# Optimization experiments

Hardware: AMD Instinct MI355X
Metric: run time of the kernel (lower is better)

## Reference

```python
import jax, jax.numpy as jnp
import numpy as np

THRESHOLD = 10.0
K = 24
EPS = 1e-9
BN_EPS = 1e-5


def setup_inputs() -> dict:
    key = jax.random.key(0)
    k0, k1, k2, k3 = jax.random.split(key, 4)
    B, C, H, W = 4, 256, 64, 64
    x = jax.random.normal(k0, (B, C, H, W), jnp.float32)
    fc_w = jax.random.normal(k1, (C, C), jnp.float32) * (1.0 / np.sqrt(C))
    fc_b = jax.random.normal(k2, (C,), jnp.float32) * 0.01
    dist_w = jax.random.normal(k3, (64, C), jnp.float32) * (1.0 / np.sqrt(C))
    bn_gamma = jnp.ones((C,), jnp.float32)
    bn_beta = jnp.zeros((C,), jnp.float32)
    return {"x": x, "fc_w": fc_w, "fc_b": fc_b, "dist_w": dist_w,
            "bn_gamma": bn_gamma, "bn_beta": bn_beta}


def reference(x, fc_w, fc_b, dist_w, bn_gamma, bn_beta):
    B, C, H, W = x.shape
    N = H * W
    # ds branch: only triggers when H == 40; here H=64 so ds=1 (no pool/interp)
    x_flat = x.reshape(B, C, N).transpose(0, 2, 1)        # [B, N, C]
    # dist_embed: 1x1 conv == linear projection per spatial location
    emb = jnp.einsum('bnc,ec->bne', x_flat, dist_w)       # [B, N, 64]
    # pairwise Euclidean distances (cdist)
    sq = jnp.sum(emb * emb, axis=-1)                      # [B, N]
    d2 = sq[:, :, None] + sq[:, None, :] - 2.0 * jnp.einsum('bne,bme->bnm', emb, emb)
    dist = jnp.sqrt(jnp.clip(d2, 0.0))                    # [B, N, N]
    # kNN mask via top_k of -dist
    _, idx = jax.lax.top_k(-dist, K)                      # [B, N, K]
    bi = jnp.arange(B)[:, None, None]
    ni = jnp.arange(N)[None, :, None]
    knn_mask = jnp.zeros((B, N, N), bool).at[bi, ni, idx].set(True)
    adj = knn_mask & (dist <= THRESHOLD)
    adj = adj | jnp.eye(N, dtype=bool)[None]
    adj_f = adj.astype(x.dtype)                           # H: [B, N, E=N]
    # HypConv: X' = Dv^{-1} H De^{-1} H^T (X Theta), residual added outside
    X_lin = x_flat @ fc_w.T + fc_b                        # [B, N, C]
    Dv = jnp.clip(jnp.sum(adj_f, axis=2), EPS, None)      # [B, N]
    De = jnp.clip(jnp.sum(adj_f, axis=1), EPS, None)      # [B, E]
    H_De_inv = adj_f / De[:, None, :]
    S = (H_De_inv @ adj_f.transpose(0, 2, 1)) / Dv[:, :, None]   # [B, N, N]
    out_flat = S @ X_lin + x_flat                         # residual
    out = out_flat.transpose(0, 2, 1).reshape(B, C, H, W)
    # BatchNorm2d in training mode (batch statistics, biased variance)
    mean = jnp.mean(out, axis=(0, 2, 3))
    var = jnp.var(out, axis=(0, 2, 3))
    o = (out - mean[None, :, None, None]) * jax.lax.rsqrt(var[None, :, None, None] + BN_EPS)
    o = o * bn_gamma[None, :, None, None] + bn_beta[None, :, None, None]
    # SiLU
    return o * jax.nn.sigmoid(o)
```

## Files before the change

kernel.cpp:

```cpp
#include <hip/hip_runtime.h>

#define NB 4096
#define BATCH 4
#define CD 256
#define ED 64
#define KNN 24

typedef __attribute__((ext_vector_type(8))) short bf16x8;
typedef __attribute__((ext_vector_type(4))) float f32x4;

__device__ __forceinline__ unsigned short f2bf(float x) {
  unsigned u = __float_as_uint(x);
  unsigned r = (u + 0x7fffu + ((u >> 16) & 1u)) >> 16;
  return (unsigned short)r;
}

__global__ __launch_bounds__(256) void k_emb(const float* __restrict__ x,
                                             const float* __restrict__ dist_w,
                                             unsigned* __restrict__ emb_hl,
                                             float* __restrict__ sq,
                                             unsigned* __restrict__ thr_g) {
  __shared__ float wds[ED * CD];
  __shared__ float red[64 * 4];
  const int b = blockIdx.x >> 6;
  const int n0 = (blockIdx.x & 63) << 6;
  const int tid = threadIdx.x;
  const float4* wsrc = (const float4*)dist_w;
  float4* wdst = (float4*)wds;
#pragma unroll
  for (int k = 0; k < 16; ++k) wdst[tid + 256 * k] = wsrc[tid + 256 * k];
  __syncthreads();
  const int eg = tid >> 6;
  const int nl = tid & 63;
  const int n = n0 + nl;
  float acc[16];
#pragma unroll
  for (int t = 0; t < 16; ++t) acc[t] = 0.f;
  const float* xb = x + (size_t)b * CD * NB + n;
#pragma unroll 2
  for (int c4 = 0; c4 < CD; c4 += 4) {
    float x0 = xb[(size_t)(c4 + 0) * NB];
    float x1 = xb[(size_t)(c4 + 1) * NB];
    float x2 = xb[(size_t)(c4 + 2) * NB];
    float x3 = xb[(size_t)(c4 + 3) * NB];
#pragma unroll
    for (int t = 0; t < 16; ++t) {
      float4 wv = *(const float4*)&wds[(eg * 16 + t) * CD + c4];
      acc[t] = fmaf(x0, wv.x, acc[t]);
      acc[t] = fmaf(x1, wv.y, acc[t]);
      acc[t] = fmaf(x2, wv.z, acc[t]);
      acc[t] = fmaf(x3, wv.w, acc[t]);
    }
  }
  float s = 0.f;
#pragma unroll
  for (int t = 0; t < 16; ++t) s = fmaf(acc[t], acc[t], s);
  unsigned hw[8], lw[8];
#pragma unroll
  for (int i = 0; i < 8; ++i) {
    unsigned short h0 = f2bf(acc[2 * i]);
    unsigned short h1 = f2bf(acc[2 * i + 1]);
    float l0f = acc[2 * i] - __uint_as_float((unsigned)h0 << 16);
    float l1f = acc[2 * i + 1] - __uint_as_float((unsigned)h1 << 16);
    hw[i] = (unsigned)h0 | ((unsigned)h1 << 16);
    lw[i] = (unsigned)f2bf(l0f) | ((unsigned)f2bf(l1f) << 16);
  }
  uint4* g = (uint4*)emb_hl;
  const size_t gb = ((size_t)(b * NB + n)) * 16;
  const int k15 = n & 15;
  g[gb + ((2 * eg) ^ k15)]     = make_uint4(hw[0], hw[1], hw[2], hw[3]);
  g[gb + ((2 * eg + 1) ^ k15)] = make_uint4(hw[4], hw[5], hw[6], hw[7]);
  g[gb + ((8 + 2 * eg) ^ k15)]     = make_uint4(lw[0], lw[1], lw[2], lw[3]);
  g[gb + ((8 + 2 * eg + 1) ^ k15)] = make_uint4(lw[4], lw[5], lw[6], lw[7]);
  red[nl * 4 + eg] = s;
  __syncthreads();
  if (tid < 64) {
    sq[b * NB + n0 + tid] = red[tid * 4] + red[tid * 4 + 1] + red[tid * 4 + 2] + red[tid * 4 + 3];
    thr_g[(b << 12) + n0 + tid] = 0x42C80000u;
  }
}

__global__ __launch_bounds__(256) void k_xlin(const float* __restrict__ x,
                                              const float* __restrict__ fc_w,
                                              const float* __restrict__ fc_b,
                                              float* __restrict__ xlin) {
  __shared__ float xt[64 * 64];
  __shared__ float wt[64 * 260];
  const int b = blockIdx.x >> 6;
  const int n0 = (blockIdx.x & 63) << 6;
  const int tid = threadIdx.x;
  const int nl4 = tid & 15;
  const int cg = tid >> 4;
  float acc[4][16];
#pragma unroll
  for (int i = 0; i < 4; ++i)
#pragma unroll
    for (int j = 0; j < 16; ++j) acc[i][j] = 0.f;

  for (int kt = 0; kt < 4; ++kt) {
    __syncthreads();
#pragma unroll 4
    for (int i = 0; i < 16; ++i) {
      int idx = tid + 256 * i;
      int k = idx >> 6, n = idx & 63;
      xt[idx] = x[((size_t)(b * CD + kt * 64 + k)) * NB + n0 + n];
    }
#pragma unroll 4
    for (int i = 0; i < 16; ++i) {
      int q = tid + 256 * i;
      int c = q >> 4, k4 = (q & 15) * 4;
      float4 v = *(const float4*)&fc_w[(size_t)c * CD + kt * 64 + k4];
      wt[(k4 + 0) * 260 + c] = v.x;
      wt[(k4 + 1) * 260 + c] = v.y;
      wt[(k4 + 2) * 260 + c] = v.z;
      wt[(k4 + 3) * 260 + c] = v.w;
    }
    __syncthreads();
#pragma unroll 2
    for (int k = 0; k < 64; ++k) {
      float4 xv = *(const float4*)&xt[k * 64 + 4 * nl4];
#pragma unroll
      for (int j = 0; j < 4; ++j) {
        float4 wv = *(const float4*)&wt[k * 260 + 4 * cg + 64 * j];
        const float* wp = &wv.x;
#pragma unroll
        for (int l = 0; l < 4; ++l) {
          acc[0][4 * j + l] = fmaf(xv.x, wp[l], acc[0][4 * j + l]);
          acc[1][4 * j + l] = fmaf(xv.y, wp[l], acc[1][4 * j + l]);
          acc[2][4 * j + l] = fmaf(xv.z, wp[l], acc[2][4 * j + l]);
          acc[3][4 * j + l] = fmaf(xv.w, wp[l], acc[3][4 * j + l]);
        }
      }
    }
  }
#pragma unroll
  for (int i = 0; i < 4; ++i) {
    int n = n0 + 4 * nl4 + i;
    float* dst = xlin + ((size_t)(b * NB + n)) * CD;
#pragma unroll
    for (int j = 0; j < 4; ++j) {
      int c = 4 * cg + 64 * j;
      float4 bv = *(const float4*)&fc_b[c];
      float4 o;
      o.x = acc[i][4 * j + 0] + bv.x;
      o.y = acc[i][4 * j + 1] + bv.y;
      o.z = acc[i][4 * j + 2] + bv.z;
      o.w = acc[i][4 * j + 3] + bv.w;
      *(float4*)&dst[c] = o;
    }
  }
}

__global__ __launch_bounds__(512, 4) void k_distp(const unsigned* __restrict__ emb_hl,
                                                  const float* __restrict__ sq,
                                                  unsigned* __restrict__ thr_g,
                                                  unsigned long long* __restrict__ part) {
  __shared__ __align__(16) unsigned char smem[78592];
  unsigned* eN = (unsigned*)smem;
  unsigned* eM = (unsigned*)(smem + 16384);
  float* sqN   = (float*)(smem + 32768);
  float* sqMp  = (float*)(smem + 33024);
  int* hist    = (int*)(smem + 35072);
  int* collectK= (int*)(smem + 51456);
  int* cnt     = (int*)(smem + 51712);
  unsigned long long* cand = (unsigned long long*)(smem + 51968);

  const int bid = blockIdx.x;
  const int mp = bid & 7;
  const int nt = (bid >> 3) & 63;
  const int b  = bid >> 9;
  const int n0 = nt << 6;
  const int m00 = mp << 9;
  const int tid = threadIdx.x;
  const uint4* embg = (const uint4*)emb_hl;
  const size_t bbase = (size_t)b * NB;
  const int gbase = (b << 12) + n0;

#pragma unroll
  for (int k = 0; k < 2; ++k) {
    int q = tid + 512 * k;
    int r = q >> 4, ch = q & 15;
    *(uint4*)&eN[r * 64 + ch * 4] = embg[(bbase + n0 + r) * 16 + ch];
  }
  if (tid < 64) sqN[tid] = sq[b * NB + n0 + tid];
  sqMp[tid] = sq[b * NB + m00 + tid];
#pragma unroll
  for (int i = 0; i < 8; ++i) hist[tid + 512 * i] = 0;

  const int w = tid >> 6, lane = tid & 63;
  const int quad = lane >> 4, lr = lane & 15;
  const int rt = w >> 1;
  const int ct0 = (w & 1) * 2;
  const int rowA = rt * 16 + lr;
  const int rA = tid >> 4, chA = tid & 15;
  const int rB = rA + 32;

  uint4 pf0, pf1;

#define CHUNK_MFMA(m0_)                                                            \
  f32x4 acc0 = {0.f, 0.f, 0.f, 0.f};                                               \
  f32x4 acc1 = {0.f, 0.f, 0.f, 0.f};                                               \
  _Pragma("unroll")                                                                \
  for (int kk = 0; kk < 2; ++kk) {                                                 \
    const int cb = quad + 4 * kk;                                                  \
    bf16x8 a_hi = *(const bf16x8*)&eN[rowA * 64 + ((cb) ^ lr) * 4];                \
    bf16x8 a_lo = *(const bf16x8*)&eN[rowA * 64 + ((cb + 8) ^ lr) * 4];            \
    int rowB0 = ct0 * 16 + lr, rowB1 = rowB0 + 16;                                 \
    bf16x8 b0_hi = *(const bf16x8*)&eM[rowB0 * 64 + ((cb) ^ lr) * 4];              \
    bf16x8 b0_lo = *(const bf16x8*)&eM[rowB0 * 64 + ((cb + 8) ^ lr) * 4];          \
    bf16x8 b1_hi = *(const bf16x8*)&eM[rowB1 * 64 + ((cb) ^ lr) * 4];              \
    bf16x8 b1_lo = *(const bf16x8*)&eM[rowB1 * 64 + ((cb + 8) ^ lr) * 4];          \
    acc0 = __builtin_amdgcn_mfma_f32_16x16x32_bf16(a_hi, b0_hi, acc0, 0, 0, 0);    \
    acc0 = __builtin_amdgcn_mfma_f32_16x16x32_bf16(a_hi, b0_lo, acc0, 0, 0, 0);    \
    acc0 = __builtin_amdgcn_mfma_f32_16x16x32_bf16(a_lo, b0_hi, acc0, 0, 0, 0);    \
    acc1 = __builtin_amdgcn_mfma_f32_16x16x32_bf16(a_hi, b1_hi, acc1, 0, 0, 0);    \
    acc1 = __builtin_amdgcn_mfma_f32_16x16x32_bf16(a_hi, b1_lo, acc1, 0, 0, 0);    \
    acc1 = __builtin_amdgcn_mfma_f32_16x16x32_bf16(a_lo, b1_hi, acc1, 0, 0, 0);    \
  }

#define STAGE_FIRST()                                                \
  pf0 = embg[(bbase + m00 + rA) * 16 + chA];                         \
  pf1 = embg[(bbase + m00 + rB) * 16 + chA];                         \
  *(uint4*)&eM[rA * 64 + chA * 4] = pf0;                             \
  *(uint4*)&eM[rB * 64 + chA * 4] = pf1;                             \
  pf0 = embg[(bbase + m00 + 64 + rA) * 16 + chA];                    \
  pf1 = embg[(bbase + m00 + 64 + rB) * 16 + chA];

#define RESTAGE(ci_, m0_)                                            \
  if ((ci_) < 7) {                                                   \
    *(uint4*)&eM[rA * 64 + chA * 4] = pf0;                           \
    *(uint4*)&eM[rB * 64 + chA * 4] = pf1;                           \
    if ((ci_) < 6) {                                                 \
      pf0 = embg[(bbase + m00 + (m0_) + 128 + rA) * 16 + chA];       \
      pf1 = embg[(bbase + m00 + (m0_) + 128 + rB) * 16 + chA];       \
    }                                                                \
  }

  STAGE_FIRST()
#pragma unroll 1
  for (int ci = 0; ci < 8; ++ci) {
    const int m0 = ci << 6;
    __syncthreads();
    CHUNK_MFMA(m0)
#pragma unroll
    for (int reg = 0; reg < 4; ++reg) {
      int row = rt * 16 + quad * 4 + reg;
      int c0 = ct0 * 16 + lr, c1 = c0 + 16;
      float d20 = fmaxf(sqN[row] + sqMp[m0 + c0] - 2.f * acc0[reg], 0.f);
      float d21 = fmaxf(sqN[row] + sqMp[m0 + c1] - 2.f * acc1[reg], 0.f);
      if (__float_as_uint(d20) <= 0x42C80000u) {
        int bk0 = min(63, (int)(d20 * 0.64f));
        atomicAdd(&hist[bk0 * 64 + row], 1);
      }
      if (__float_as_uint(d21) <= 0x42C80000u) {
        int bk1 = min(63, (int)(d21 * 0.64f));
        atomicAdd(&hist[bk1 * 64 + row], 1);
      }
    }
    __syncthreads();
    RESTAGE(ci, m0)
  }

  if (tid < 64) {
    int cum = 0, kb = 63;
#pragma unroll 1
    for (int k2 = 0; k2 < 64; ++k2) {
      cum += hist[k2 * 64 + tid];
      if (cum >= 24) { kb = k2; break; }
    }
    float edge = (float)(kb + 2) * 1.5625f;
    atomicMin(&thr_g[gbase + tid], __float_as_uint(edge));
    unsigned tg = thr_g[gbase + tid];
    int kImp = min(63, (int)(__uint_as_float(tg) * 0.64f));
    collectK[tid] = min(kb, kImp);
    cnt[tid] = 0;
  }
#pragma unroll
  for (int i = 0; i < 7; ++i) {
    int q = tid + 512 * i;
    if (q < 64 * 52) cand[q] = ~0ULL;
  }
  __syncthreads();

  STAGE_FIRST()
#pragma unroll 1
  for (int ci = 0; ci < 8; ++ci) {
    const int m0 = ci << 6;
    __syncthreads();
    CHUNK_MFMA(m0)
#pragma unroll
    for (int reg = 0; reg < 4; ++reg) {
      int row = rt * 16 + quad * 4 + reg;
      int c0 = ct0 * 16 + lr, c1 = c0 + 16;
      float d20 = fmaxf(sqN[row] + sqMp[m0 + c0] - 2.f * acc0[reg], 0.f);
      float d21 = fmaxf(sqN[row] + sqMp[m0 + c1] - 2.f * acc1[reg], 0.f);
      int kc = collectK[row];
      unsigned bi0 = __float_as_uint(d20), bi1 = __float_as_uint(d21);
      int bk0 = min(63, (int)(d20 * 0.64f));
      int bk1 = min(63, (int)(d21 * 0.64f));
      if (bk0 <= kc && bi0 <= 0x42C80000u) {
        int pos = atomicAdd(&cnt[row], 1);
        if (pos < 52) cand[row * 52 + pos] = ((unsigned long long)bi0 << 32) | (unsigned)(m00 + m0 + c0);
      }
      if (bk1 <= kc && bi1 <= 0x42C80000u) {
        int pos = atomicAdd(&cnt[row], 1);
        if (pos < 52) cand[row * 52 + pos] = ((unsigned long long)bi1 << 32) | (unsigned)(m00 + m0 + c1);
      }
    }
    __syncthreads();
    RESTAGE(ci, m0)
  }
  __syncthreads();

  {
    const int row8 = tid >> 3, sub = tid & 7;
    unsigned long long last = 0;
    unsigned long long* op = part + ((size_t)bid * 64 + row8) * 24;
#pragma unroll 1
    for (int k = 0; k < 24; ++k) {
      unsigned long long lm = ~0ULL;
#pragma unroll
      for (int j2 = 0; j2 < 7; ++j2) {
        int p2 = sub + 8 * j2;
        if (p2 < 52) {
          unsigned long long v2 = cand[row8 * 52 + p2];
          if ((k == 0 || v2 > last) && v2 < lm) lm = v2;
        }
      }
#pragma unroll
      for (int s2 = 1; s2 < 8; s2 <<= 1) {
        unsigned long long o2 = __shfl_xor(lm, s2);
        if (o2 < lm) lm = o2;
      }
      if (sub == 0) op[k] = lm;
      last = lm;
    }
  }
}

__global__ __launch_bounds__(256) void k_merge(const unsigned long long* __restrict__ part,
                                               int* __restrict__ row_idx,
                                               int* __restrict__ row_cnt,
                                               int* __restrict__ col_cnt) {
  const int row = blockIdx.x * 256 + threadIdx.x;
  const int b = row >> 12;
  const int n = row & 4095;
  const int nt = n >> 6, r = n & 63;
  const size_t gb = (size_t)(((b << 6) | nt) << 3);
  unsigned long long h[8];
  int pp[8];
#pragma unroll
  for (int t = 0; t < 8; ++t) {
    h[t] = part[((gb + t) * 64 + r) * 24];
    pp[t] = 0;
  }
  int cnt = 0;
  const int base = row * KNN;
  for (int k = 0; k < 24; ++k) {
    int bs = 0;
    unsigned long long mv = h[0];
#pragma unroll
    for (int t = 1; t < 8; ++t)
      if (h[t] < mv) { mv = h[t]; bs = t; }
    if ((unsigned)(mv >> 32) > 0x42C80000u) break;
    int mi = (int)(mv & 0xFFFFFFFFu);
    row_idx[base + cnt] = mi;
    atomicAdd(&col_cnt[(b << 12) + mi], 1);
    ++cnt;
    int np = ++pp[bs];
    h[bs] = (np < 24) ? part[((gb + bs) * 64 + r) * 24 + np] : ~0ULL;
  }
  row_cnt[row] = cnt;
#pragma unroll 4
  for (int j = cnt; j < 24; ++j) row_idx[base + j] = n;
}

__global__ __launch_bounds__(256) void k_scan(const int* __restrict__ col_cnt,
                                              int* __restrict__ col_start,
                                              int* __restrict__ col_cursor) {
  __shared__ int part[256];
  const int tid = threadIdx.x;
  const int base = tid * 64;
  int s = 0;
  for (int j = 0; j < 64; ++j) s += col_cnt[base + j];
  part[tid] = s;
  __syncthreads();
  for (int off = 1; off < 256; off <<= 1) {
    int v = (tid >= off) ? part[tid - off] : 0;
    __syncthreads();
    part[tid] += v;
    __syncthreads();
  }
  int run = part[tid] - s;
  for (int j = 0; j < 64; ++j) {
    col_start[base + j] = run;
    col_cursor[base + j] = run;
    run += col_cnt[base + j];
  }
}

__global__ __launch_bounds__(256) void k_fill(const int* __restrict__ row_idx,
                                              const int* __restrict__ row_cnt,
                                              int* __restrict__ col_cursor,
                                              int* __restrict__ col_list) {
  const int row = blockIdx.x * 256 + threadIdx.x;
  const int b = row >> 12;
  const int cnt = row_cnt[row];
  for (int j = 0; j < cnt; ++j) {
    int m = row_idx[row * KNN + j];
    int pos = atomicAdd(&col_cursor[(b << 12) + m], 1);
    col_list[pos] = row & 4095;
  }
}

__global__ __launch_bounds__(256) void k_yd(const float* __restrict__ xlin,
                                            const int* __restrict__ col_cnt,
                                            const int* __restrict__ col_start,
                                            const int* __restrict__ col_list,
                                            float* __restrict__ yd) {
  const int le = threadIdx.x >> 6;
  const int c4 = threadIdx.x & 63;
  const int be = blockIdx.x * 4 + le;
  const int b = be >> 12;
  const int deg = col_cnt[be];
  const int start = col_start[be];
  float4 acc = make_float4(0.f, 0.f, 0.f, 0.f);
  int j = 0;
  for (; j + 3 < deg; j += 4) {
    int ma = col_list[start + j], mb2 = col_list[start + j + 1];
    int mc = col_list[start + j + 2], md = col_list[start + j + 3];
    float4 va = *(const float4*)&xlin[(((size_t)(b << 12) + ma) << 8) + c4 * 4];
    float4 vb = *(const float4*)&xlin[(((size_t)(b << 12) + mb2) << 8) + c4 * 4];
    float4 vc = *(const float4*)&xlin[(((size_t)(b << 12) + mc) << 8) + c4 * 4];
    float4 vd = *(const float4*)&xlin[(((size_t)(b << 12) + md) << 8) + c4 * 4];
    acc.x += (va.x + vb.x) + (vc.x + vd.x);
    acc.y += (va.y + vb.y) + (vc.y + vd.y);
    acc.z += (va.z + vb.z) + (vc.z + vd.z);
    acc.w += (va.w + vb.w) + (vc.w + vd.w);
  }
  for (; j < deg; ++j) {
    int m = col_list[start + j];
    float4 v = *(const float4*)&xlin[(((size_t)(b << 12) + m) << 8) + c4 * 4];
    acc.x += v.x; acc.y += v.y; acc.z += v.z; acc.w += v.w;
  }
  float inv = 1.f / (float)deg;
  acc.x *= inv; acc.y *= inv; acc.z *= inv; acc.w *= inv;
  *(float4*)&yd[((size_t)be << 8) + c4 * 4] = acc;
}

__global__ __launch_bounds__(256) void k_out2(const float* __restrict__ yd,
                                              const int* __restrict__ row_idx,
                                              const int* __restrict__ row_cnt,
                                              float* __restrict__ outf) {
  const int b = blockIdx.x >> 8;
  const int nt = blockIdx.x & 255;
  const int le = threadIdx.x >> 6;
  const int c4 = threadIdx.x & 63;
  for (int ii = 0; ii < 4; ++ii) {
    int n = nt * 16 + le * 4 + ii;
    int row = (b << 12) + n;
    int cnt = row_cnt[row];
    int idx[24];
    const int4* ip = (const int4*)(row_idx + (size_t)row * KNN);
#pragma unroll
    for (int t = 0; t < 6; ++t) {
      int4 v = ip[t];
      idx[4 * t] = v.x; idx[4 * t + 1] = v.y; idx[4 * t + 2] = v.z; idx[4 * t + 3] = v.w;
    }
    float4 acc = make_float4(0.f, 0.f, 0.f, 0.f);
#pragma unroll
    for (int j = 0; j < 24; ++j) {
      float wgt = (j < cnt) ? 1.f : 0.f;
      float4 v = *(const float4*)&yd[(((size_t)(b << 12) + idx[j]) << 8) + c4 * 4];
      acc.x = fmaf(wgt, v.x, acc.x);
      acc.y = fmaf(wgt, v.y, acc.y);
      acc.z = fmaf(wgt, v.z, acc.z);
      acc.w = fmaf(wgt, v.w, acc.w);
    }
    float inv = 1.f / (float)cnt;
    acc.x *= inv; acc.y *= inv; acc.z *= inv; acc.w *= inv;
    *(float4*)&outf[((size_t)row << 8) + c4 * 4] = acc;
  }
}

__global__ __launch_bounds__(256) void k_res_bn(const float* __restrict__ x,
                                                float* __restrict__ outf,
                                                float* __restrict__ bn_sum,
                                                float* __restrict__ bn_sumsq) {
  __shared__ float xt[256 * 69];
  const int b = blockIdx.x >> 6;
  const int n0 = (blockIdx.x & 63) << 6;
  const int tid = threadIdx.x;
#pragma unroll 4
  for (int k = 0; k < 16; ++k) {
    int q = tid + 256 * k;
    int c = q >> 4, f = q & 15;
    float4 v = *(const float4*)&x[((size_t)(b * CD + c)) * NB + n0 + 4 * f];
    xt[c * 69 + 4 * f + 0] = v.x;
    xt[c * 69 + 4 * f + 1] = v.y;
    xt[c * 69 + 4 * f + 2] = v.z;
    xt[c * 69 + 4 * f + 3] = v.w;
  }
  __syncthreads();
  float s = 0.f, q = 0.f;
  const size_t rbase = ((size_t)((b << 12) + n0)) << 8;
#pragma unroll 4
  for (int i = 0; i < 64; ++i) {
    float v = outf[rbase + (size_t)i * 256 + tid] + xt[tid * 69 + i];
    outf[rbase + (size_t)i * 256 + tid] = v;
    s += v;
    q = fmaf(v, v, q);
  }
  atomicAdd(&bn_sum[tid], s);
  atomicAdd(&bn_sumsq[tid], q);
}

__global__ __launch_bounds__(256) void k_bn(const float* __restrict__ bn_sum,
                                            const float* __restrict__ bn_sumsq,
                                            const float* __restrict__ gamma,
                                            const float* __restrict__ beta,
                                            float* __restrict__ scale,
                                            float* __restrict__ shift) {
  const int c = threadIdx.x;
  const float inv = 1.f / 16384.f;
  float mean = bn_sum[c] * inv;
  float var = bn_sumsq[c] * inv - mean * mean;
  float sc = gamma[c] * rsqrtf(var + 1e-5f);
  scale[c] = sc;
  shift[c] = beta[c] - mean * sc;
}

__global__ __launch_bounds__(256) void k_write(const float* __restrict__ outf,
                                               const float* __restrict__ scale,
                                               const float* __restrict__ shift,
                                               float* __restrict__ out) {
  __shared__ float tile[64 * 257];
  __shared__ float sc[256], sh[256];
  const int b = blockIdx.x >> 6;
  const int n0 = (blockIdx.x & 63) << 6;
  const int tid = threadIdx.x;
  sc[tid] = scale[tid];
  sh[tid] = shift[tid];
  __syncthreads();
#pragma unroll 4
  for (int i = 0; i < 64; ++i) {
    int idx = tid + 256 * i;
    int n = idx >> 8, c = idx & 255;
    float v = outf[(((size_t)(b << 12) + n0 + n) << 8) + c];
    v = fmaf(v, sc[c], sh[c]);
    float w = v / (1.f + expf(-v));
    tile[n * 257 + c] = w;
  }
  __syncthreads();
  const int nl = tid & 63;
  const int cg = tid >> 6;
#pragma unroll 4
  for (int j = 0; j < 64; ++j) {
    int c = cg * 64 + j;
    out[((size_t)(b * CD + c)) * NB + n0 + nl] = tile[nl * 257 + c];
  }
}

extern "C" void kernel_launch(void* const* d_in, const int* in_sizes, int n_in,
                              void* d_out, int out_size, void* d_ws, size_t ws_size,
                              hipStream_t stream) {
  const float* x      = (const float*)d_in[0];
  const float* fc_w   = (const float*)d_in[1];
  const float* fc_b   = (const float*)d_in[2];
  const float* dist_w = (const float*)d_in[3];
  const float* gamma  = (const float*)d_in[4];
  const float* beta   = (const float*)d_in[5];
  float* out = (float*)d_out;
  char* ws = (char*)d_ws;

  const size_t OFF_EHL   = 0;
  const size_t OFF_XLIN  = (size_t)4 << 20;
  const size_t OFF_YD    = (size_t)20 << 20;
  const size_t OFF_OUTF  = (size_t)36 << 20;
  const size_t OFF_SQ    = (size_t)52 << 20;
  const size_t OFF_RIDX  = OFF_SQ + 65536;
  const size_t OFF_RCNT  = OFF_RIDX + 1572864;
  const size_t OFF_CCNT  = OFF_RCNT + 65536;
  const size_t OFF_CSTART = OFF_CCNT + 65536;
  const size_t OFF_CCUR  = OFF_CSTART + 65536;
  const size_t OFF_CLIST = OFF_CCUR + 65536;
  const size_t OFF_BNS   = OFF_CLIST + 1572864;
  const size_t OFF_BNQ   = OFF_BNS + 1024;
  const size_t OFF_SCALE = OFF_BNQ + 1024;
  const size_t OFF_SHIFT = OFF_SCALE + 1024;
  const size_t OFF_THRG  = OFF_SHIFT + 1024;
  const size_t TOTAL = OFF_THRG + 65536;
  if (ws_size < TOTAL) return;

  unsigned* emb_hl = (unsigned*)(ws + OFF_EHL);
  float* xlin  = (float*)(ws + OFF_XLIN);
  float* yd    = (float*)(ws + OFF_YD);
  float* outf  = (float*)(ws + OFF_OUTF);
  unsigned long long* part = (unsigned long long*)(ws + OFF_YD);
  float* sq    = (float*)(ws + OFF_SQ);
  int* row_idx = (int*)(ws + OFF_RIDX);
  int* row_cnt = (int*)(ws + OFF_RCNT);
  int* col_cnt = (int*)(ws + OFF_CCNT);
  int* col_start = (int*)(ws + OFF_CSTART);
  int* col_cursor = (int*)(ws + OFF_CCUR);
  int* col_list = (int*)(ws + OFF_CLIST);
  float* bn_sum = (float*)(ws + OFF_BNS);
  float* bn_sumsq = (float*)(ws + OFF_BNQ);
  float* scale = (float*)(ws + OFF_SCALE);
  float* shift = (float*)(ws + OFF_SHIFT);
  unsigned* thr_g = (unsigned*)(ws + OFF_THRG);

  hipMemsetAsync(col_cnt, 0, 65536, stream);
  hipMemsetAsync(bn_sum, 0, 2048, stream);

  k_emb<<<256, 256, 0, stream>>>(x, dist_w, emb_hl, sq, thr_g);
  k_xlin<<<256, 256, 0, stream>>>(x, fc_w, fc_b, xlin);
  k_distp<<<2048, 512, 0, stream>>>(emb_hl, sq, thr_g, part);
  k_merge<<<64, 256, 0, stream>>>(part, row_idx, row_cnt, col_cnt);
  k_scan<<<1, 256, 0, stream>>>(col_cnt, col_start, col_cursor);
  k_fill<<<64, 256, 0, stream>>>(row_idx, row_cnt, col_cursor, col_list);
  k_yd<<<4096, 256, 0, stream>>>(xlin, col_cnt, col_start, col_list, yd);
  k_out2<<<1024, 256, 0, stream>>>(yd, row_idx, row_cnt, outf);
  k_res_bn<<<256, 256, 0, stream>>>(x, outf, bn_sum, bn_sumsq);
  k_bn<<<1, 256, 0, stream>>>(bn_sum, bn_sumsq, gamma, beta, scale, shift);
  k_write<<<256, 256, 0, stream>>>(outf, scale, shift, out);
}
```

Measured before the change: 527.7 us.

## Move X·W GEMM to split-bf16 MFMA, shrink merge/fill blocks, fuse BN into write

The fp32 SIMT GEMM that computes X_lin is replaced by MFMA bf16 instructions on hi/lo split operands (three products per tile), with a new kernel that pre-splits fc_w and more blocks across output-channel tiles. k_merge and k_fill now run with 64-thread blocks so their 16K rows spread over more CUs. The separate k_bn launch is removed and each k_write block computes scale and shift itself. The bf16x3 split gives up a little accuracy compared with full fp32 and adds one small launch.

After: 497.5 us. 1.06x faster.

```diff
diff --git a/kernel.cpp b/kernel.cpp
--- a/kernel.cpp
+++ b/kernel.cpp
@@ -80,74 +80,113 @@
   }
 }
 
-__global__ __launch_bounds__(256) void k_xlin(const float* __restrict__ x,
-                                              const float* __restrict__ fc_w,
+__global__ __launch_bounds__(256) void k_wsplit(const float* __restrict__ fc_w,
+                                                unsigned* __restrict__ w_hl) {
+  const int u = blockIdx.x * 256 + threadIdx.x;
+  const int c = u >> 5, cg = u & 31;
+  const int kt = cg >> 3, chl = cg & 7;
+  const float* src = fc_w + (size_t)c * CD + kt * 64 + chl * 8;
+  unsigned hi[4], lo[4];
+#pragma unroll
+  for (int j = 0; j < 4; ++j) {
+    float a0 = src[2 * j], a1 = src[2 * j + 1];
+    unsigned short h0 = f2bf(a0), h1 = f2bf(a1);
+    float l0 = a0 - __uint_as_float((unsigned)h0 << 16);
+    float l1 = a1 - __uint_as_float((unsigned)h1 << 16);
+    hi[j] = (unsigned)h0 | ((unsigned)h1 << 16);
+    lo[j] = (unsigned)f2bf(l0) | ((unsigned)f2bf(l1) << 16);
+  }
+  uint4* dst = (uint4*)w_hl;
+  const int base = (c * 4 + kt) * 16;
+  const int k15 = c & 15;
+  dst[base + (chl ^ k15)] = make_uint4(hi[0], hi[1], hi[2], hi[3]);
+  dst[base + ((chl + 8) ^ k15)] = make_uint4(lo[0], lo[1], lo[2], lo[3]);
+}
+
+__global__ __launch_bounds__(512) void k_xlin(const float* __restrict__ x,
+                                              const unsigned* __restrict__ w_hl,
                                               const float* __restrict__ fc_b,
                                               float* __restrict__ xlin) {
-  __shared__ float xt[64 * 64];
-  __shared__ float wt[64 * 260];
-  const int b = blockIdx.x >> 6;
-  const int n0 = (blockIdx.x & 63) << 6;
+  __shared__ __align__(16) unsigned char smem[49152];
+  float* xt = (float*)smem;
+  unsigned* xhl = (unsigned*)(smem + 16384);
+  unsigned* whl = (unsigned*)(smem + 32768);
+  const int bid = blockIdx.x;
+  const int ct = bid & 3;
+  const int nt = (bid >> 2) & 63;
+  const int b = bid >> 8;
+  const int n0 = nt << 6;
   const int tid = threadIdx.x;
-  const int nl4 = tid & 15;
-  const int cg = tid >> 4;
-  float acc[4][16];
-#pragma unroll
-  for (int i = 0; i < 4; ++i)
-#pragma unroll
-    for (int j = 0; j < 16; ++j) acc[i][j] = 0.f;
-
+  const int w = tid >> 6, lane = tid & 63;
+  const int quad = lane >> 4, lr = lane & 15;
+  const int rt = w >> 1;
+  const int ct0 = (w & 1) * 2;
+  const int rowA = rt * 16 + lr;
+  const int cvt_n = tid & 63, cvt_k8 = tid >> 6;
+  uint4* whl4 = (uint4*)whl;
+  uint4* xhl4 = (uint4*)xhl;
+  const uint4* wg = (const uint4*)w_hl;
+  f32x4 acc0 = {0.f, 0.f, 0.f, 0.f};
+  f32x4 acc1 = {0.f, 0.f, 0.f, 0.f};
+
+#pragma unroll 1
   for (int kt = 0; kt < 4; ++kt) {
     __syncthreads();
-#pragma unroll 4
-    for (int i = 0; i < 16; ++i) {
-      int idx = tid + 256 * i;
+#pragma unroll
+    for (int i = 0; i < 8; ++i) {
+      int idx = tid + 512 * i;
       int k = idx >> 6, n = idx & 63;
-      xt[idx] = x[((size_t)(b * CD + kt * 64 + k)) * NB + n0 + n];
-    }
-#pragma unroll 4
-    for (int i = 0; i < 16; ++i) {
-      int q = tid + 256 * i;
-      int c = q >> 4, k4 = (q & 15) * 4;
-      float4 v = *(const float4*)&fc_w[(size_t)c * CD + kt * 64 + k4];
-      wt[(k4 + 0) * 260 + c] = v.x;
-      wt[(k4 + 1) * 260 + c] = v.y;
-      wt[(k4 + 2) * 260 + c] = v.z;
-      wt[(k4 + 3) * 260 + c] = v.w;
-    }
-    __syncthreads();
-#pragma unroll 2
-    for (int k = 0; k < 64; ++k) {
-      float4 xv = *(const float4*)&xt[k * 64 + 4 * nl4];
+      xt[k * 64 + n] = x[((size_t)(b * CD + kt * 64 + k)) * NB + n0 + n];
+    }
+#pragma unroll
+    for (int i = 0; i < 2; ++i) {
+      int idx = tid + 512 * i;
+      int r = idx >> 4, ch = idx & 15;
+      whl4[r * 16 + ch] = wg[(size_t)((ct * 64 + r) * 4 + kt) * 16 + ch];
+    }
+    __syncthreads();
+    {
+      unsigned hi[4], lo[4];
 #pragma unroll
       for (int j = 0; j < 4; ++j) {
-        float4 wv = *(const float4*)&wt[k * 260 + 4 * cg + 64 * j];
-        const float* wp = &wv.x;
-#pragma unroll
-        for (int l = 0; l < 4; ++l) {
-          acc[0][4 * j + l] = fmaf(xv.x, wp[l], acc[0][4 * j + l]);
-          acc[1][4 * j + l] = fmaf(xv.y, wp[l], acc[1][4 * j + l]);
-          acc[2][4 * j + l] = fmaf(xv.z, wp[l], acc[2][4 * j + l]);
-          acc[3][4 * j + l] = fmaf(xv.w, wp[l], acc[3][4 * j + l]);
-        }
+        float a0 = xt[(cvt_k8 * 8 + 2 * j) * 64 + cvt_n];
+        float a1 = xt[(cvt_k8 * 8 + 2 * j + 1) * 64 + cvt_n];
+        unsigned short h0 = f2bf(a0), h1 = f2bf(a1);
+        float l0 = a0 - __uint_as_float((unsigned)h0 << 16);
+        float l1 = a1 - __uint_as_float((unsigned)h1 << 16);
+        hi[j] = (unsigned)h0 | ((unsigned)h1 << 16);
+        lo[j] = (unsigned)f2bf(l0) | ((unsigned)f2bf(l1) << 16);
       }
-    }
-  }
-#pragma unroll
-  for (int i = 0; i < 4; ++i) {
-    int n = n0 + 4 * nl4 + i;
-    float* dst = xlin + ((size_t)(b * NB + n)) * CD;
-#pragma unroll
-    for (int j = 0; j < 4; ++j) {
-      int c = 4 * cg + 64 * j;
-      float4 bv = *(const float4*)&fc_b[c];
-      float4 o;
-      o.x = acc[i][4 * j + 0] + bv.x;
-      o.y = acc[i][4 * j + 1] + bv.y;
-      o.z = acc[i][4 * j + 2] + bv.z;
-      o.w = acc[i][4 * j + 3] + bv.w;
-      *(float4*)&dst[c] = o;
-    }
+      const int k15 = cvt_n & 15;
+      xhl4[cvt_n * 16 + (cvt_k8 ^ k15)] = make_uint4(hi[0], hi[1], hi[2], hi[3]);
+      xhl4[cvt_n * 16 + ((cvt_k8 + 8) ^ k15)] = make_uint4(lo[0], lo[1], lo[2], lo[3]);
+    }
+    __syncthreads();
+#pragma unroll
+    for (int kk = 0; kk < 2; ++kk) {
+      const int cb = quad + 4 * kk;
+      bf16x8 a_hi = *(const bf16x8*)&xhl[rowA * 64 + ((cb) ^ lr) * 4];
+      bf16x8 a_lo = *(const bf16x8*)&xhl[rowA * 64 + ((cb + 8) ^ lr) * 4];
+      int rowB0 = ct0 * 16 + lr, rowB1 = rowB0 + 16;
+      bf16x8 b0_hi = *(const bf16x8*)&whl[rowB0 * 64 + ((cb) ^ lr) * 4];
+      bf16x8 b0_lo = *(const bf16x8*)&whl[rowB0 * 64 + ((cb + 8) ^ lr) * 4];
+      bf16x8 b1_hi = *(const bf16x8*)&whl[rowB1 * 64 + ((cb) ^ lr) * 4];
+      bf16x8 b1_lo = *(const bf16x8*)&whl[rowB1 * 64 + ((cb + 8) ^ lr) * 4];
+      acc0 = __builtin_amdgcn_mfma_f32_16x16x32_bf16(a_hi, b0_hi, acc0, 0, 0, 0);
+      acc0 = __builtin_amdgcn_mfma_f32_16x16x32_bf16(a_hi, b0_lo, acc0, 0, 0, 0);
+      acc0 = __builtin_amdgcn_mfma_f32_16x16x32_bf16(a_lo, b0_hi, acc0, 0, 0, 0);
+      acc1 = __builtin_amdgcn_mfma_f32_16x16x32_bf16(a_hi, b1_hi, acc1, 0, 0, 0);
+      acc1 = __builtin_amdgcn_mfma_f32_16x16x32_bf16(a_hi, b1_lo, acc1, 0, 0, 0);
+      acc1 = __builtin_amdgcn_mfma_f32_16x16x32_bf16(a_lo, b1_hi, acc1, 0, 0, 0);
+    }
+  }
+#pragma unroll
+  for (int reg = 0; reg < 4; ++reg) {
+    int n = n0 + rt * 16 + quad * 4 + reg;
+    float* dst = xlin + ((size_t)(b * NB + n)) * CD + ct * 64;
+    int c0 = ct0 * 16 + lr;
+    dst[c0] = acc0[reg] + fc_b[ct * 64 + c0];
+    dst[c0 + 16] = acc1[reg] + fc_b[ct * 64 + c0 + 16];
   }
 }
 
@@ -338,11 +377,11 @@
   }
 }
 
-__global__ __launch_bounds__(256) void k_merge(const unsigned long long* __restrict__ part,
-                                               int* __restrict__ row_idx,
-                                               int* __restrict__ row_cnt,
-                                               int* __restrict__ col_cnt) {
-  const int row = blockIdx.x * 256 + threadIdx.x;
+__global__ __launch_bounds__(64) void k_merge(const unsigned long long* __restrict__ part,
+                                              int* __restrict__ row_idx,
+                                              int* __restrict__ row_cnt,
+                                              int* __restrict__ col_cnt) {
+  const int row = blockIdx.x * 64 + threadIdx.x;
   const int b = row >> 12;
   const int n = row & 4095;
   const int nt = n >> 6, r = n & 63;
@@ -399,11 +438,11 @@
   }
 }
 
-__global__ __launch_bounds__(256) void k_fill(const int* __restrict__ row_idx,
-                                              const int* __restrict__ row_cnt,
-                                              int* __restrict__ col_cursor,
-                                              int* __restrict__ col_list) {
-  const int row = blockIdx.x * 256 + threadIdx.x;
+__global__ __launch_bounds__(64) void k_fill(const int* __restrict__ row_idx,
+                                             const int* __restrict__ row_cnt,
+                                             int* __restrict__ col_cursor,
+                                             int* __restrict__ col_list) {
+  const int row = blockIdx.x * 64 + threadIdx.x;
   const int b = row >> 12;
   const int cnt = row_cnt[row];
   for (int j = 0; j < cnt; ++j) {
@@ -515,32 +554,25 @@
   atomicAdd(&bn_sumsq[tid], q);
 }
 
-__global__ __launch_bounds__(256) void k_bn(const float* __restrict__ bn_sum,
-                                            const float* __restrict__ bn_sumsq,
-                                            const float* __restrict__ gamma,
-                                            const float* __restrict__ beta,
-                                            float* __restrict__ scale,
-                                            float* __restrict__ shift) {
-  const int c = threadIdx.x;
-  const float inv = 1.f / 16384.f;
-  float mean = bn_sum[c] * inv;
-  float var = bn_sumsq[c] * inv - mean * mean;
-  float sc = gamma[c] * rsqrtf(var + 1e-5f);
-  scale[c] = sc;
-  shift[c] = beta[c] - mean * sc;
-}
-
 __global__ __launch_bounds__(256) void k_write(const float* __restrict__ outf,
-                                               const float* __restrict__ scale,
-                                               const float* __restrict__ shift,
+                                               const float* __restrict__ bn_sum,
+                                               const float* __restrict__ bn_sumsq,
+                                               const float* __restrict__ gamma,
+                                               const float* __restrict__ beta,
                                                float* __restrict__ out) {
   __shared__ float tile[64 * 257];
   __shared__ float sc[256], sh[256];
   const int b = blockIdx.x >> 6;
   const int n0 = (blockIdx.x & 63) << 6;
   const int tid = threadIdx.x;
-  sc[tid] = scale[tid];
-  sh[tid] = shift[tid];
+  {
+    const float inv = 1.f / 16384.f;
+    float mean = bn_sum[tid] * inv;
+    float var = bn_sumsq[tid] * inv - mean * mean;
+    float scf = gamma[tid] * rsqrtf(var + 1e-5f);
+    sc[tid] = scf;
+    sh[tid] = beta[tid] - mean * scf;
+  }
   __syncthreads();
 #pragma unroll 4
   for (int i = 0; i < 64; ++i) {
@@ -586,10 +618,9 @@
   const size_t OFF_CLIST = OFF_CCUR + 65536;
   const size_t OFF_BNS   = OFF_CLIST + 1572864;
   const size_t OFF_BNQ   = OFF_BNS + 1024;
-  const size_t OFF_SCALE = OFF_BNQ + 1024;
-  const size_t OFF_SHIFT = OFF_SCALE + 1024;
-  const size_t OFF_THRG  = OFF_SHIFT + 1024;
-  const size_t TOTAL = OFF_THRG + 65536;
+  const size_t OFF_THRG  = OFF_BNQ + 1024;
+  const size_t OFF_WHL   = OFF_THRG + 65536;
+  const size_t TOTAL = OFF_WHL + 262144;
   if (ws_size < TOTAL) return;
 
   unsigned* emb_hl = (unsigned*)(ws + OFF_EHL);
@@ -606,22 +637,21 @@
   int* col_list = (int*)(ws + OFF_CLIST);
   float* bn_sum = (float*)(ws + OFF_BNS);
   float* bn_sumsq = (float*)(ws + OFF_BNQ);
-  float* scale = (float*)(ws + OFF_SCALE);
-  float* shift = (float*)(ws + OFF_SHIFT);
   unsigned* thr_g = (unsigned*)(ws + OFF_THRG);
+  unsigned* w_hl = (unsigned*)(ws + OFF_WHL);
 
   hipMemsetAsync(col_cnt, 0, 65536, stream);
   hipMemsetAsync(bn_sum, 0, 2048, stream);
 
   k_emb<<<256, 256, 0, stream>>>(x, dist_w, emb_hl, sq, thr_g);
-  k_xlin<<<256, 256, 0, stream>>>(x, fc_w, fc_b, xlin);
+  k_wsplit<<<32, 256, 0, stream>>>(fc_w, w_hl);
+  k_xlin<<<1024, 512, 0, stream>>>(x, w_hl, fc_b, xlin);
   k_distp<<<2048, 512, 0, stream>>>(emb_hl, sq, thr_g, part);
-  k_merge<<<64, 256, 0, stream>>>(part, row_idx, row_cnt, col_cnt);
+  k_merge<<<256, 64, 0, stream>>>(part, row_idx, row_cnt, col_cnt);
   k_scan<<<1, 256, 0, stream>>>(col_cnt, col_start, col_cursor);
-  k_fill<<<64, 256, 0, stream>>>(row_idx, row_cnt, col_cursor, col_list);
+  k_fill<<<256, 64, 0, stream>>>(row_idx, row_cnt, col_cursor, col_list);
   k_yd<<<4096, 256, 0, stream>>>(xlin, col_cnt, col_start, col_list, yd);
   k_out2<<<1024, 256, 0, stream>>>(yd, row_idx, row_cnt, outf);
   k_res_bn<<<256, 256, 0, stream>>>(x, outf, bn_sum, bn_sumsq);
-  k_bn<<<1, 256, 0, stream>>>(bn_sum, bn_sumsq, gamma, beta, scale, shift);
-  k_write<<<256, 256, 0, stream>>>(outf, scale, shift, out);
-}
+  k_write<<<256, 256, 0, stream>>>(outf, bn_sum, bn_sumsq, gamma, beta, out);
+}
```
